# Kernel tuning notes

Measured on AMD Instinct MI355X. Metric: run time of the kernel, lower is better.

The kernel has to match this reference:

```python
import jax, jax.numpy as jnp
import numpy as np

V, E, H, T, B = 100000, 256, 512, 160, 256
FORGET_BIAS = 2.0


def peephole_lstm(x_emb, lengths, W, b, w_i, w_f, w_o):
    """TF LSTMCell(use_peepholes=True) + dynamic_rnn sequence_length semantics.
    x_emb: [B,T,E] float32, lengths: [B] int32. Returns final hidden state h [B,H].
    Gate order matches TF: i, j(cell), f, o.
    """
    Bsz = x_emb.shape[0]
    Hd = w_i.shape[0]
    c0 = jnp.zeros((Bsz, Hd), x_emb.dtype)
    h0 = jnp.zeros((Bsz, Hd), x_emb.dtype)

    def step(carry, inputs):
        c, h = carry
        x_t, t = inputs
        z = jnp.concatenate([x_t, h], axis=-1) @ W + b          # [B, 4H]
        zi, zj, zf, zo = jnp.split(z, 4, axis=-1)
        i = jax.nn.sigmoid(zi + w_i * c)
        f = jax.nn.sigmoid(zf + FORGET_BIAS + w_f * c)
        c_new = f * c + i * jnp.tanh(zj)
        o = jax.nn.sigmoid(zo + w_o * c_new)
        h_new = o * jnp.tanh(c_new)
        m = (t < lengths)[:, None]                               # freeze state past length
        return (jnp.where(m, c_new, c), jnp.where(m, h_new, h)), None

    xs = jnp.swapaxes(x_emb, 0, 1)                               # [T,B,E]
    ts = jnp.arange(xs.shape[0], dtype=jnp.int32)
    (c, h), _ = jax.lax.scan(step, (c0, h0), (xs, ts))
    return h


def setup_inputs() -> dict:
    key = jax.random.key(0)
    ks = jax.random.split(key, 10)
    input_queries = jax.random.randint(ks[0], (B, T), 0, V, dtype=jnp.int32)
    input_replies = jax.random.randint(ks[1], (B, T), 0, V, dtype=jnp.int32)
    query_lengths = jax.random.randint(ks[2], (B,), 1, T + 1, dtype=jnp.int32)
    reply_lengths = jax.random.randint(ks[3], (B,), 1, T + 1, dtype=jnp.int32)
    s = 1.0 / np.sqrt(E + H)
    embeddings = jax.random.normal(ks[4], (V, E), jnp.float32) * 0.1
    W = jax.random.normal(ks[5], (E + H, 4 * H), jnp.float32) * s
    b = jnp.zeros((4 * H,), jnp.float32)
    w_i = jax.random.normal(ks[6], (H,), jnp.float32) * 0.1
    w_f = jax.random.normal(ks[7], (H,), jnp.float32) * 0.1
    w_o = jax.random.normal(ks[8], (H,), jnp.float32) * 0.1
    M = jax.random.truncated_normal(ks[9], -2.0, 2.0, (H, H), jnp.float32)
    return {
        "input_queries": input_queries, "input_replies": input_replies,
        "query_lengths": query_lengths, "reply_lengths": reply_lengths,
        "embeddings": embeddings, "W": W, "b": b,
        "w_i": w_i, "w_f": w_f, "w_o": w_o, "M": M,
    }


def reference(input_queries, input_replies, query_lengths, reply_lengths,
              embeddings, W, b, w_i, w_f, w_o, M):
    q_emb = embeddings[input_queries]                            # [B,T,E]
    r_emb = embeddings[input_replies]                            # [B,T,E]
    # reply cell is created with reuse=True -> shares weights with query cell
    q_enc = peephole_lstm(q_emb, query_lengths, W, b, w_i, w_f, w_o)   # [B,H]
    r_enc = peephole_lstm(r_emb, reply_lengths, W, b, w_i, w_f, w_o)   # [B,H]
    e_enc = peephole_lstm(q_emb, query_lengths, W, b, w_i, w_f, w_o)   # echo: queries thru shared cell
    q_proj = q_enc @ M                                           # dense_layer
    distances = q_proj @ r_enc.T                                 # [B,B] in-batch scores
    echo_distances = q_proj @ e_enc.T                            # [B,B]
    positive_logits = jnp.diagonal(distances)                    # eye mask gather
    return distances, echo_distances, positive_logits
```

## Files before the change

### kernel.cpp

```cpp
#include <hip/hip_runtime.h>
#include <math.h>

#define TT 160
#define EE 256
#define HH 512
#define KK 768
#define B2 512
#define BQ 256
#define N4 2048

typedef __attribute__((ext_vector_type(8)))  _Float16 half8;
typedef __attribute__((ext_vector_type(16))) float f32x16;

__device__ inline unsigned short f2h(float x){ union{_Float16 h; unsigned short u;}v; v.h=(_Float16)x; return v.u; }
__device__ inline float h2f(unsigned short u){ union{_Float16 h; unsigned short u;}v; v.u=u; return (float)v.h; }
__device__ inline unsigned int packh2(float a,float b){ union{_Float16 h[2]; unsigned int u;}v; v.h[0]=(_Float16)a; v.h[1]=(_Float16)b; return v.u; }

#define LOG2E 1.44269504088896f
__device__ inline float sigmf(float x){
    return __builtin_amdgcn_rcpf(1.0f + __builtin_amdgcn_exp2f(-LOG2E * x));
}
__device__ inline float tanhfast(float x){
    return 1.0f - 2.0f * __builtin_amdgcn_rcpf(__builtin_amdgcn_exp2f(2.0f * LOG2E * x) + 1.0f);
}

__device__ inline void gload_lds16_c(const void* g, void* l){
    __builtin_amdgcn_global_load_lds(
        (const __attribute__((address_space(1))) void*)g,
        (__attribute__((address_space(3))) void*)l, 16, 0, 0);
}
__device__ inline void gload_lds16_sc(const void* g, void* l){
    __builtin_amdgcn_global_load_lds(
        (const __attribute__((address_space(1))) void*)g,
        (__attribute__((address_space(3))) void*)l, 16, 0, 0x11);
}

__global__ __launch_bounds__(256) void transposeW(const float* __restrict__ W,
                                                  unsigned short* __restrict__ Wt) {
    __shared__ float tile[32][33];
    const int tx = threadIdx.x & 31, ty = threadIdx.x >> 5;
    const int cb = blockIdx.x * 32;
    const int kb = blockIdx.y * 32;
    #pragma unroll
    for (int j = 0; j < 4; j++)
        tile[ty + j * 8][tx] = W[(size_t)(kb + ty + j * 8) * N4 + cb + tx];
    __syncthreads();
    #pragma unroll
    for (int j = 0; j < 4; j++) {
        int cl = ty + j * 8;
        int col = cb + cl;
        int gate = col >> 9, unit = col & 511;
        Wt[(size_t)(unit * 4 + gate) * KK + kb + tx] = f2h(tile[tx][cl]);
    }
}

__global__ __launch_bounds__(256) void xprep(const float* __restrict__ emb,
                                             const int* __restrict__ qids,
                                             const int* __restrict__ rids,
                                             unsigned short* __restrict__ xseq) {
    const int widx = blockIdx.x * 4 + (threadIdx.x >> 6);
    const int lane = threadIdx.x & 63;
    const int row  = widx & 511;
    const int t    = widx >> 9;
    const int id   = (row < BQ) ? qids[row * TT + t] : rids[(row - BQ) * TT + t];
    const float4 f = *(const float4*)&emb[(size_t)id * EE + lane * 4];
    *(uint2*)&xseq[(size_t)widx * EE + lane * 4] =
        make_uint2(packh2(f.x, f.y), packh2(f.z, f.w));
}

__global__ __launch_bounds__(256, 1)
__attribute__((amdgpu_waves_per_eu(1, 1)))
void lstm_persist(
    const unsigned short* __restrict__ Wt,
    const unsigned short* __restrict__ xseq,
    const float* __restrict__ bias,
    const float* __restrict__ wi_, const float* __restrict__ wf_,
    const float* __restrict__ wo_,
    const int* __restrict__ qlen, const int* __restrict__ rlen,
    unsigned short* __restrict__ hbA, unsigned short* __restrict__ hbB,
    unsigned int* __restrict__ bar)
{
    extern __shared__ char smem[];
    float* zb = (float*)(smem + 98304);

    const int tid = threadIdx.x;
    const int bid = blockIdx.x;
    const int g   = bid & 7;
    const int bc  = bid >> 3;
    const int rb  = g * 64;
    unsigned int* gflags = bar + g * 64;
    const int l = tid & 63, w = tid >> 6;
    const int wr = w >> 1, wc = w & 1;

    half8 wfrag[48];
    {
        const int colp = bc * 64 + wc * 32 + (l & 31);
        const unsigned short* wrow = Wt + (size_t)colp * KK + (l >> 5) * 8;
        #pragma unroll
        for (int f = 0; f < 48; f++) wfrag[f] = *(const half8*)(wrow + 16 * f);
    }

    const int erow = tid >> 2;
    const int eu   = (tid & 3) << 2;
    const int Ug0  = bc * 16 + eu;
    const float4 b_i = *(const float4*)&bias[Ug0];
    const float4 b_j = *(const float4*)&bias[HH + Ug0];
    const float4 b_f = *(const float4*)&bias[2 * HH + Ug0];
    const float4 b_o = *(const float4*)&bias[3 * HH + Ug0];
    const float4 wiv = *(const float4*)&wi_[Ug0];
    const float4 wfv = *(const float4*)&wf_[Ug0];
    const float4 wov = *(const float4*)&wo_[Ug0];
    const int len = (rb + erow < BQ) ? qlen[rb + erow] : rlen[rb + erow - BQ];
    float cc[4] = {0.f,0.f,0.f,0.f}, hh[4] = {0.f,0.f,0.f,0.f};

    auto stage = [&](int tk, int tt, const unsigned short* hsrc) {
        char* base = smem + tk * 16384;
        #pragma unroll
        for (int i2 = 0; i2 < 4; i2++) {
            const int rowbase = w * 16 + i2 * 4;
            const int row = rowbase + (l >> 4);
            const int cch = l & 15;
            const int srcElem = (cch ^ (row & 15)) << 3;
            if (tk < 2) {
                const unsigned short* src =
                    xseq + ((size_t)(tt * B2 + rb + row) * EE + tk * 128 + srcElem);
                gload_lds16_c(src, base + rowbase * 256);
            } else {
                const unsigned short* src =
                    hsrc + ((size_t)(rb + row) * HH + (tk - 2) * 128 + srcElem);
                gload_lds16_sc(src, base + rowbase * 256);
            }
        }
    };

    auto compute = [&](int tk, f32x16* a0, f32x16* a1) {
        const char* Ab = smem + tk * 16384;
        const int ra = wr * 32 + (l & 31);
        const int kg = l >> 5;
        #pragma unroll
        for (int f8 = 0; f8 < 8; f8++) {
            const int kc = f8 * 2 + kg;
            half8 av = *(const half8*)(Ab + ra * 256 + (((kc ^ (ra & 15)) << 3) * 2));
            if (f8 & 1) *a1 = __builtin_amdgcn_mfma_f32_32x32x16_f16(av, wfrag[tk * 8 + f8], *a1, 0, 0, 0);
            else        *a0 = __builtin_amdgcn_mfma_f32_32x32x16_f16(av, wfrag[tk * 8 + f8], *a0, 0, 0, 0);
        }
    };

    stage(0, 0, hbA);
    stage(1, 0, hbA);
    __syncthreads();

    #pragma unroll 1
    for (int t = 0; t < TT; t++) {
        const unsigned short* hbp = (t & 1) ? hbB : hbA;
        unsigned short* hbq       = (t & 1) ? hbA : hbB;
        f32x16 acc0 = {0,0,0,0,0,0,0,0,0,0,0,0,0,0,0,0};
        f32x16 acc1 = {0,0,0,0,0,0,0,0,0,0,0,0,0,0,0,0};

        compute(0, &acc0, &acc1);
        compute(1, &acc0, &acc1);
        if (t > 0 && tid < 32) {
            while (__hip_atomic_load(&gflags[tid], __ATOMIC_RELAXED,
                                     __HIP_MEMORY_SCOPE_AGENT) < (unsigned)t)
                __builtin_amdgcn_s_sleep(1);
        }
        __syncthreads();

        stage(2, t, hbp);
        stage(3, t, hbp);
        stage(4, t, hbp);
        stage(5, t, hbp);
        if (t < TT - 1) {
            stage(0, t + 1, hbp);
            stage(1, t + 1, hbp);
        }
        __syncthreads();

        compute(2, &acc0, &acc1);
        compute(3, &acc0, &acc1);
        compute(4, &acc0, &acc1);
        compute(5, &acc0, &acc1);

        {
            const int colb = wc * 32 + (l & 31);
            const int c4i = colb >> 2, cr = colb & 3;
            const f32x16 s = acc0 + acc1;
            #pragma unroll
            for (int r = 0; r < 16; r++) {
                const int row = wr * 32 + 4 * (l >> 5) + (r & 3) + 8 * (r >> 2);
                zb[row * 64 + ((c4i ^ (row & 15)) << 2) + cr] = s[r];
            }
        }
        __syncthreads();

        {
            if (t < len) {
                #pragma unroll
                for (int j = 0; j < 4; j++) {
                    const float4 z4 = *(const float4*)
                        &zb[erow * 64 + (((eu + j) ^ (erow & 15)) << 2)];
                    const float cp = cc[j];
                    const float ig = sigmf(z4.x + (&b_i.x)[j] + (&wiv.x)[j] * cp);
                    const float jg = tanhfast(z4.y + (&b_j.x)[j]);
                    const float fg = sigmf(z4.z + (&b_f.x)[j] + 2.0f + (&wfv.x)[j] * cp);
                    const float cn = fg * cp + ig * jg;
                    const float og = sigmf(z4.w + (&b_o.x)[j] + (&wov.x)[j] * cn);
                    cc[j] = cn;
                    hh[j] = og * tanhfast(cn);
                }
            }
            union { unsigned short s[4]; unsigned long long v; } pk;
            #pragma unroll
            for (int j = 0; j < 4; j++) pk.s[j] = f2h(hh[j]);
            __hip_atomic_store(
                (unsigned long long*)&hbq[(size_t)(rb + erow) * HH + Ug0], pk.v,
                __ATOMIC_RELAXED, __HIP_MEMORY_SCOPE_AGENT);
        }
        __syncthreads();

        if (t < TT - 1 && tid == 0)
            __hip_atomic_store(&gflags[bc], (unsigned)(t + 1),
                               __ATOMIC_RELAXED, __HIP_MEMORY_SCOPE_AGENT);
    }
}

__global__ __launch_bounds__(512) void proj_kernel(
    const unsigned short* __restrict__ h, const float* __restrict__ M,
    float* __restrict__ qp)
{
    const int i = blockIdx.x;
    const int j = threadIdx.x;
    float s = 0.0f;
    for (int k = 0; k < HH; k++) s += h2f(h[(size_t)i * HH + k]) * M[(size_t)k * HH + j];
    qp[(size_t)i * HH + j] = s;
}

__global__ __launch_bounds__(256) void nt_gemm(
    const float* __restrict__ A,
    const unsigned short* __restrict__ B0, const unsigned short* __restrict__ B1,
    float* __restrict__ C0, float* __restrict__ C1)
{
    const unsigned short* Bm = blockIdx.z ? B1 : B0;
    float* Cm                = blockIdx.z ? C1 : C0;
    __shared__ float sA[16][17];
    __shared__ float sB[16][17];
    const int ti = threadIdx.x >> 4;
    const int tj = threadIdx.x & 15;
    const int ib = blockIdx.y * 16;
    const int jb = blockIdx.x * 16;
    float acc = 0.0f;
    for (int kk = 0; kk < HH; kk += 16) {
        sA[ti][tj] = A[(size_t)(ib + ti) * HH + kk + tj];
        sB[ti][tj] = h2f(Bm[(size_t)(jb + ti) * HH + kk + tj]);
        __syncthreads();
        #pragma unroll
        for (int k = 0; k < 16; k++) acc += sA[ti][k] * sB[tj][k];
        __syncthreads();
    }
    Cm[(size_t)(ib + ti) * 256 + jb + tj] = acc;
}

__global__ void diag_kernel(const float* __restrict__ dist, float* __restrict__ pos) {
    int i = threadIdx.x;
    pos[i] = dist[(size_t)i * 256 + i];
}

extern "C" void kernel_launch(void* const* d_in, const int* in_sizes, int n_in,
                              void* d_out, int out_size, void* d_ws, size_t ws_size,
                              hipStream_t stream) {
    const int*   qids = (const int*)d_in[0];
    const int*   rids = (const int*)d_in[1];
    const int*   qlen = (const int*)d_in[2];
    const int*   rlen = (const int*)d_in[3];
    const float* emb  = (const float*)d_in[4];
    const float* W    = (const float*)d_in[5];
    const float* bias = (const float*)d_in[6];
    const float* wi   = (const float*)d_in[7];
    const float* wf   = (const float*)d_in[8];
    const float* wo   = (const float*)d_in[9];
    const float* M    = (const float*)d_in[10];

    float* out       = (float*)d_out;
    float* distances = out;
    float* echo      = out + 256 * 256;
    float* pos       = out + 2 * 256 * 256;

    char* ws = (char*)d_ws;
    unsigned short* Wt   = (unsigned short*)(ws);
    unsigned short* xseq = (unsigned short*)(ws + 3145728);
    unsigned short* hbA  = (unsigned short*)(ws + 45088768);
    unsigned short* hbB  = (unsigned short*)(ws + 45613056);
    float*          qp   = (float*)(ws + 46137344);
    unsigned int*   bar  = (unsigned int*)(ws + 46661632);

    const int SMEM = 114688;
    hipFuncSetAttribute((const void*)lstm_persist,
                        hipFuncAttributeMaxDynamicSharedMemorySize, SMEM);

    transposeW<<<dim3(64, 24), dim3(256), 0, stream>>>(W, Wt);
    xprep<<<dim3(TT * B2 / 4), dim3(256), 0, stream>>>(emb, qids, rids, xseq);
    hipMemsetAsync(hbA, 0, 524288, stream);
    hipMemsetAsync(bar, 0, 4096, stream);

    lstm_persist<<<dim3(256), dim3(256), SMEM, stream>>>(
        Wt, xseq, bias, wi, wf, wo, qlen, rlen, hbA, hbB, bar);

    proj_kernel<<<dim3(256), dim3(512), 0, stream>>>(hbA, M, qp);
    nt_gemm<<<dim3(16, 16, 2), dim3(256), 0, stream>>>(
        qp, hbA + (size_t)BQ * HH , hbA , distances, echo);
    diag_kernel<<<dim3(1), dim3(256), 0, stream>>>(distances, pos);
}
```

Baseline: 686.8 us.

## Split LSTM recurrence K-dimension across two wave groups in persistent kernel

Doubles the persistent LSTM block to 512 threads. Each pair of waves now splits the K reduction in half, so each wave holds 24 weight fragments instead of 48. Each half writes partial gate sums to its own LDS buffer, and the pointwise step adds the two halves. The aim is to halve the serial MFMA chain per wave on each timestep of the latency-bound recurrence and spread the staging and pointwise work over more waves. The cost is extra LDS (128KB), a second partial-sum read and add, and more threads taking part in each barrier.

```diff
diff --git a/kernel.cpp b/kernel.cpp
--- a/kernel.cpp
+++ b/kernel.cpp
@@ -68,9 +68,7 @@
         make_uint2(packh2(f.x, f.y), packh2(f.z, f.w));
 }
 
-__global__ __launch_bounds__(256, 1)
-__attribute__((amdgpu_waves_per_eu(1, 1)))
-void lstm_persist(
+__global__ __launch_bounds__(512, 1) void lstm_persist(
     const unsigned short* __restrict__ Wt,
     const unsigned short* __restrict__ xseq,
     const float* __restrict__ bias,
@@ -81,7 +79,8 @@
     unsigned int* __restrict__ bar)
 {
     extern __shared__ char smem[];
-    float* zb = (float*)(smem + 98304);
+    float* zb0 = (float*)(smem + 98304);
+    float* zb1 = zb0 + 4096;
 
     const int tid = threadIdx.x;
     const int bid = blockIdx.x;
@@ -90,34 +89,37 @@
     const int rb  = g * 64;
     unsigned int* gflags = bar + g * 64;
     const int l = tid & 63, w = tid >> 6;
-    const int wr = w >> 1, wc = w & 1;
-
-    half8 wfrag[48];
+    const int wr = (w >> 2) & 1, wc = (w >> 1) & 1, kg = w & 1;
+
+    half8 wfrag[24];
     {
         const int colp = bc * 64 + wc * 32 + (l & 31);
-        const unsigned short* wrow = Wt + (size_t)colp * KK + (l >> 5) * 8;
+        const unsigned short* wrow = Wt + (size_t)colp * KK + kg * 64 + (l >> 5) * 8;
         #pragma unroll
-        for (int f = 0; f < 48; f++) wfrag[f] = *(const half8*)(wrow + 16 * f);
+        for (int c = 0; c < 6; c++)
+            #pragma unroll
+            for (int f4 = 0; f4 < 4; f4++)
+                wfrag[c * 4 + f4] = *(const half8*)(wrow + c * 128 + f4 * 16);
     }
 
-    const int erow = tid >> 2;
-    const int eu   = (tid & 3) << 2;
-    const int Ug0  = bc * 16 + eu;
-    const float4 b_i = *(const float4*)&bias[Ug0];
-    const float4 b_j = *(const float4*)&bias[HH + Ug0];
-    const float4 b_f = *(const float4*)&bias[2 * HH + Ug0];
-    const float4 b_o = *(const float4*)&bias[3 * HH + Ug0];
-    const float4 wiv = *(const float4*)&wi_[Ug0];
-    const float4 wfv = *(const float4*)&wf_[Ug0];
-    const float4 wov = *(const float4*)&wo_[Ug0];
+    const int erow = tid >> 3;
+    const int eu0  = (tid & 7) * 2;
+    const int Ug0  = bc * 16 + eu0;
+    const float bi0 = bias[Ug0],        bi1 = bias[Ug0 + 1];
+    const float bj0 = bias[HH + Ug0],   bj1 = bias[HH + Ug0 + 1];
+    const float bf0 = bias[2*HH + Ug0], bf1 = bias[2*HH + Ug0 + 1];
+    const float bo0 = bias[3*HH + Ug0], bo1 = bias[3*HH + Ug0 + 1];
+    const float wi0 = wi_[Ug0], wi1 = wi_[Ug0 + 1];
+    const float wf0 = wf_[Ug0], wf1 = wf_[Ug0 + 1];
+    const float wo0 = wo_[Ug0], wo1 = wo_[Ug0 + 1];
     const int len = (rb + erow < BQ) ? qlen[rb + erow] : rlen[rb + erow - BQ];
-    float cc[4] = {0.f,0.f,0.f,0.f}, hh[4] = {0.f,0.f,0.f,0.f};
+    float cc[2] = {0.f, 0.f}, hh[2] = {0.f, 0.f};
 
     auto stage = [&](int tk, int tt, const unsigned short* hsrc) {
         char* base = smem + tk * 16384;
         #pragma unroll
-        for (int i2 = 0; i2 < 4; i2++) {
-            const int rowbase = w * 16 + i2 * 4;
+        for (int i2 = 0; i2 < 2; i2++) {
+            const int rowbase = w * 8 + i2 * 4;
             const int row = rowbase + (l >> 4);
             const int cch = l & 15;
             const int srcElem = (cch ^ (row & 15)) << 3;
@@ -136,13 +138,12 @@
     auto compute = [&](int tk, f32x16* a0, f32x16* a1) {
         const char* Ab = smem + tk * 16384;
         const int ra = wr * 32 + (l & 31);
-        const int kg = l >> 5;
         #pragma unroll
-        for (int f8 = 0; f8 < 8; f8++) {
-            const int kc = f8 * 2 + kg;
-            half8 av = *(const half8*)(Ab + ra * 256 + (((kc ^ (ra & 15)) << 3) * 2));
-            if (f8 & 1) *a1 = __builtin_amdgcn_mfma_f32_32x32x16_f16(av, wfrag[tk * 8 + f8], *a1, 0, 0, 0);
-            else        *a0 = __builtin_amdgcn_mfma_f32_32x32x16_f16(av, wfrag[tk * 8 + f8], *a0, 0, 0, 0);
+        for (int f4 = 0; f4 < 4; f4++) {
+            const int kc = kg * 8 + f4 * 2 + (l >> 5);
+            half8 av = *(const half8*)(Ab + ra * 256 + ((kc ^ (ra & 15)) << 4));
+            if (f4 & 1) *a1 = __builtin_amdgcn_mfma_f32_32x32x16_f16(av, wfrag[tk * 4 + f4], *a1, 0, 0, 0);
+            else        *a0 = __builtin_amdgcn_mfma_f32_32x32x16_f16(av, wfrag[tk * 4 + f4], *a0, 0, 0, 0);
         }
     };
 
@@ -182,13 +183,14 @@
         compute(5, &acc0, &acc1);
 
         {
+            float* zbk = kg ? zb1 : zb0;
             const int colb = wc * 32 + (l & 31);
             const int c4i = colb >> 2, cr = colb & 3;
             const f32x16 s = acc0 + acc1;
             #pragma unroll
             for (int r = 0; r < 16; r++) {
                 const int row = wr * 32 + 4 * (l >> 5) + (r & 3) + 8 * (r >> 2);
-                zb[row * 64 + ((c4i ^ (row & 15)) << 2) + cr] = s[r];
+                zbk[row * 64 + ((c4i ^ (row & 15)) << 2) + cr] = s[r];
             }
         }
         __syncthreads();
@@ -196,25 +198,29 @@
         {
             if (t < len) {
                 #pragma unroll
-                for (int j = 0; j < 4; j++) {
-                    const float4 z4 = *(const float4*)
-                        &zb[erow * 64 + (((eu + j) ^ (erow & 15)) << 2)];
+                for (int j = 0; j < 2; j++) {
+                    const int u = eu0 + j;
+                    const int zoff = erow * 64 + ((u ^ (erow & 15)) << 2);
+                    const float4 za = *(const float4*)&zb0[zoff];
+                    const float4 zc = *(const float4*)&zb1[zoff];
+                    const float zi = za.x + zc.x, zj = za.y + zc.y;
+                    const float zf = za.z + zc.z, zo = za.w + zc.w;
                     const float cp = cc[j];
-                    const float ig = sigmf(z4.x + (&b_i.x)[j] + (&wiv.x)[j] * cp);
-                    const float jg = tanhfast(z4.y + (&b_j.x)[j]);
-                    const float fg = sigmf(z4.z + (&b_f.x)[j] + 2.0f + (&wfv.x)[j] * cp);
+                    const float bi = j ? bi1 : bi0, bj = j ? bj1 : bj0;
+                    const float bf = j ? bf1 : bf0, bo = j ? bo1 : bo0;
+                    const float wiv = j ? wi1 : wi0, wfv = j ? wf1 : wf0, wov = j ? wo1 : wo0;
+                    const float ig = sigmf(zi + bi + wiv * cp);
+                    const float jg = tanhfast(zj + bj);
+                    const float fg = sigmf(zf + bf + 2.0f + wfv * cp);
                     const float cn = fg * cp + ig * jg;
-                    const float og = sigmf(z4.w + (&b_o.x)[j] + (&wov.x)[j] * cn);
+                    const float og = sigmf(zo + bo + wov * cn);
                     cc[j] = cn;
                     hh[j] = og * tanhfast(cn);
                 }
             }
-            union { unsigned short s[4]; unsigned long long v; } pk;
-            #pragma unroll
-            for (int j = 0; j < 4; j++) pk.s[j] = f2h(hh[j]);
-            __hip_atomic_store(
-                (unsigned long long*)&hbq[(size_t)(rb + erow) * HH + Ug0], pk.v,
-                __ATOMIC_RELAXED, __HIP_MEMORY_SCOPE_AGENT);
+            __hip_atomic_store((unsigned int*)&hbq[(size_t)(rb + erow) * HH + Ug0],
+                               packh2(hh[0], hh[1]),
+                               __ATOMIC_RELAXED, __HIP_MEMORY_SCOPE_AGENT);
         }
         __syncthreads();
 
@@ -293,7 +299,7 @@
     float*          qp   = (float*)(ws + 46137344);
     unsigned int*   bar  = (unsigned int*)(ws + 46661632);
 
-    const int SMEM = 114688;
+    const int SMEM = 131072;
     hipFuncSetAttribute((const void*)lstm_persist,
                         hipFuncAttributeMaxDynamicSharedMemorySize, SMEM);
 
@@ -302,7 +308,7 @@
     hipMemsetAsync(hbA, 0, 524288, stream);
     hipMemsetAsync(bar, 0, 4096, stream);
 
-    lstm_persist<<<dim3(256), dim3(256), SMEM, stream>>>(
+    lstm_persist<<<dim3(256), dim3(512), SMEM, stream>>>(
         Wt, xseq, bias, wi, wf, wo, qlen, rlen, hbA, hbB, bar);
 
     proj_kernel<<<dim3(256), dim3(512), 0, stream>>>(hbA, M, qp);
```

After: 580.9 us, median of 3. 15.4% less time.
